# Optimization experiments

Measured on AMD Instinct MI355X. Metric: run time of the kernel, lower is better.

The kernel has to match this reference:

```python
import jax, jax.numpy as jnp
import numpy as np

N_NODES = 20000
N_EDGES = 640000
D = 64        # node / edge feature dim
H = 128       # MLP hidden dim


def setup_inputs() -> dict:
    key = jax.random.key(0)
    ks = jax.random.split(key, 12)
    inp = {
        "x": jax.random.normal(ks[0], (N_NODES, D), dtype=jnp.float32),
        "edge_index": jax.random.randint(ks[1], (2, N_EDGES), 0, N_NODES, dtype=jnp.int64),
        "edge_attr": jax.random.normal(ks[2], (N_EDGES, D), dtype=jnp.float32),
        "f": jax.random.normal(ks[3], (N_NODES, D), dtype=jnp.float32),
        # edge MLP: concat(x_src, x_dest, edge_attr) = 3D -> H -> D
        "We1": jax.random.normal(ks[4], (3 * D, H), dtype=jnp.float32) / np.sqrt(3 * D),
        "be1": jnp.zeros((H,), dtype=jnp.float32),
        "We2": jax.random.normal(ks[5], (H, D), dtype=jnp.float32) / np.sqrt(H),
        "be2": jnp.zeros((D,), dtype=jnp.float32),
        # node MLP: concat(x, agg, f) = 3D -> H -> D
        "Wn1": jax.random.normal(ks[6], (3 * D, H), dtype=jnp.float32) / np.sqrt(3 * D),
        "bn1": jnp.zeros((H,), dtype=jnp.float32),
        "Wn2": jax.random.normal(ks[7], (H, D), dtype=jnp.float32) / np.sqrt(H),
        "bn2": jnp.zeros((D,), dtype=jnp.float32),
    }
    return inp


def reference(x, edge_index, edge_attr, f, We1, be1, We2, be2, Wn1, bn1, Wn2, bn2):
    src, dest = edge_index[0], edge_index[1]
    # edge model: MLP over gathered src/dest node features + edge attrs
    e_in = jnp.concatenate([x[src], x[dest], edge_attr], axis=-1)      # [E, 3D]
    e_h = jax.nn.relu(e_in @ We1 + be1)                                 # [E, H]
    edge_out = e_h @ We2 + be2                                          # [E, D]
    # node model: scatter-add edge messages to dest, then MLP
    agg = jax.ops.segment_sum(edge_out, dest, num_segments=N_NODES)    # [N, D]
    n_in = jnp.concatenate([x, agg, f], axis=-1)                        # [N, 3D]
    n_h = jax.nn.relu(n_in @ Wn1 + bn1)                                 # [N, H]
    x_out = n_h @ Wn2 + bn2                                             # [N, D]
    return (x_out, edge_out)
```

## Files before the change

### kernel.cpp

```cpp
#include <hip/hip_runtime.h>

#define NE 640000
#define NN 20000
#define SEI 200
#define SEH 136
#define SEO 68

typedef __attribute__((ext_vector_type(8))) short s16x8;
typedef __attribute__((ext_vector_type(4))) short s16x4;
typedef __attribute__((ext_vector_type(4))) float f32x4;

typedef const __attribute__((ext_vector_type(4))) float cf32x4;

__device__ __forceinline__ short f2bf(float f) {
  unsigned int u = __float_as_uint(f);
  u += 0x7fffu + ((u >> 16) & 1u);
  return (short)(u >> 16);
}

__device__ __forceinline__ s16x8 cvt8(f32x4 a, f32x4 b) {
  s16x8 o;
  o[0]=f2bf(a[0]); o[1]=f2bf(a[1]); o[2]=f2bf(a[2]); o[3]=f2bf(a[3]);
  o[4]=f2bf(b[0]); o[5]=f2bf(b[1]); o[6]=f2bf(b[2]); o[7]=f2bf(b[3]);
  return o;
}

__device__ __forceinline__ void load_wfrags_lds(const float* W1, const float* W2,
                                                const float* b1, const float* b2,
                                                short* smem, int t,
                                                int wv, int r, int g,
                                                s16x8 w1f[2][6], s16x8 w2f[4],
                                                f32x4 b1r[2], f32x4* b2r) {
  #pragma unroll
  for (int i = 0; i < 24; ++i) {
    int idx4 = t + i * 256;
    f32x4 v = ((cf32x4*)W1)[idx4];
    s16x4 pk; pk[0]=f2bf(v[0]); pk[1]=f2bf(v[1]); pk[2]=f2bf(v[2]); pk[3]=f2bf(v[3]);
    *(s16x4*)&smem[idx4 * 4] = pk;
  }
  __syncthreads();
  #pragma unroll
  for (int nn = 0; nn < 2; ++nn) {
    const int h = (wv*2+nn)*16 + r;
    #pragma unroll
    for (int kk = 0; kk < 6; ++kk) {
      s16x8 wf;
      #pragma unroll
      for (int i = 0; i < 8; ++i) wf[i] = smem[(kk*32 + g*8 + i)*128 + h];
      w1f[nn][kk] = wf;
    }
    b1r[nn] = *(cf32x4*)(b1 + (wv*2+nn)*16 + g*4);
  }
  __syncthreads();
  #pragma unroll
  for (int i = 0; i < 8; ++i) {
    int idx4 = t + i * 256;
    f32x4 v = ((cf32x4*)W2)[idx4];
    s16x4 pk; pk[0]=f2bf(v[0]); pk[1]=f2bf(v[1]); pk[2]=f2bf(v[2]); pk[3]=f2bf(v[3]);
    *(s16x4*)&smem[idx4 * 4] = pk;
  }
  __syncthreads();
  {
    const int h2 = wv*16 + r;
    #pragma unroll
    for (int kk = 0; kk < 4; ++kk) {
      s16x8 wf;
      #pragma unroll
      for (int i = 0; i < 8; ++i) wf[i] = smem[(kk*32 + g*8 + i)*64 + h2];
      w2f[kk] = wf;
    }
    *b2r = *(cf32x4*)(b2 + wv*16 + g*4);
  }
  __syncthreads();
}


__global__ void count_kernel(const int* __restrict__ eidx, int* __restrict__ cursor,
                             float* __restrict__ agg) {
  const int4* d4 = (const int4*)(eidx + NE);
  int i = blockIdx.x * blockDim.x + threadIdx.x;
  if (i < NE / 4) {
    int4 d = d4[i];
    atomicAdd(&cursor[d.x], 1);
    atomicAdd(&cursor[d.y], 1);
    atomicAdd(&cursor[d.z], 1);
    atomicAdd(&cursor[d.w], 1);
  }
  if (i < NN * 64 / 8) {
    f32x4 z = {0.f, 0.f, 0.f, 0.f};
    ((f32x4*)agg)[i*2]   = z;
    ((f32x4*)agg)[i*2+1] = z;
  }
}

__global__ __launch_bounds__(1024)
void scan_kernel(int* __restrict__ cursor, int* __restrict__ offs) {
  __shared__ int cnt[20480];
  __shared__ int part[1024];
  const int t = threadIdx.x;
  for (int i = t; i < 20480; i += 1024)
    cnt[i] = (i < NN) ? cursor[i] : 0;
  __syncthreads();
  const int lo = t * 20;
  int s = 0;
  #pragma unroll
  for (int k = 0; k < 20; ++k) s += cnt[lo + k];
  part[t] = s;
  __syncthreads();
  for (int d = 1; d < 1024; d <<= 1) {
    int u = (t >= d) ? part[t - d] : 0;
    __syncthreads();
    part[t] += u;
    __syncthreads();
  }
  int run = part[t] - s;
  #pragma unroll
  for (int k = 0; k < 20; ++k) {
    int c = cnt[lo + k];
    cnt[lo + k] = run;
    run += c;
  }
  __syncthreads();
  for (int i = t; i < NN; i += 1024) {
    int v = cnt[i];
    offs[i] = v;
    cursor[i] = v;
  }
  if (t == 1023) offs[NN] = NE;
}

__global__ void scatter_kernel(const int* __restrict__ eidx,
                               int* __restrict__ cursor, int* __restrict__ elist) {
  const int4* d4 = (const int4*)(eidx + NE);
  int i = blockIdx.x * blockDim.x + threadIdx.x;
  if (i < NE / 4) {
    int4 d = d4[i];
    const int e = i * 4;
    elist[atomicAdd(&cursor[d.x], 1)] = e;
    elist[atomicAdd(&cursor[d.y], 1)] = e + 1;
    elist[atomicAdd(&cursor[d.z], 1)] = e + 2;
    elist[atomicAdd(&cursor[d.w], 1)] = e + 3;
  }
}

#define LOAD_ROWS(sv, dv, ee) do {                                        \
    cf32x4* ps_ = (cf32x4*)(x  + (size_t)(sv)*64 + p*16);                 \
    cf32x4* pd_ = (cf32x4*)(x  + (size_t)(dv)*64 + p*16);                 \
    cf32x4* pe_ = (cf32x4*)(ea + (size_t)(ee)*64 + p*16);                 \
    L[0]=ps_[0]; L[1]=ps_[1]; L[2]=ps_[2];  L[3]=ps_[3];                  \
    L[4]=pd_[0]; L[5]=pd_[1]; L[6]=pd_[2];  L[7]=pd_[3];                  \
    L[8]=pe_[0]; L[9]=pe_[1]; L[10]=pe_[2]; L[11]=pe_[3];                 \
  } while (0)

#define WRITE_EIN(buf) do {                                               \
    short* stg_ = (buf) + el*SEI + p*16;                                  \
    ((s16x8*)stg_)[0]       = cvt8(L[0], L[1]);                           \
    ((s16x8*)stg_)[1]       = cvt8(L[2], L[3]);                           \
    ((s16x8*)(stg_+64))[0]  = cvt8(L[4], L[5]);                           \
    ((s16x8*)(stg_+64))[1]  = cvt8(L[6], L[7]);                           \
    ((s16x8*)(stg_+128))[0] = cvt8(L[8], L[9]);                           \
    ((s16x8*)(stg_+128))[1] = cvt8(L[10], L[11]);                         \
  } while (0)

__global__ __launch_bounds__(256, 2)
void edge_kernel(const float* __restrict__ x, const int* __restrict__ eidx,
                 const float* __restrict__ ea, const int* __restrict__ elist,
                 const float* __restrict__ We1, const float* __restrict__ be1,
                 const float* __restrict__ We2, const float* __restrict__ be2,
                 float* __restrict__ edge_out, float* __restrict__ agg)
{
  __shared__ __align__(16) char smem[69632];
  short* sEin0 = (short*)smem;
  short* sEin1 = (short*)(smem + 25600);
  short* sEh   = (short*)(smem + 51200);
  int* sDest0  = (int*)(smem + 68608);
  int* sDest1  = (int*)(smem + 68864);
  int* sEid0   = (int*)(smem + 69120);
  int* sEid1   = (int*)(smem + 69376);

  const int t = threadIdx.x;
  const int wv = t >> 6, lane = t & 63;
  const int r = lane & 15, g = lane >> 4;

  s16x8 w1f[2][6], w2f[4];
  f32x4 b1r[2], b2r;
  load_wfrags_lds(We1, We2, be1, be2, (short*)smem, t, wv, r, g,
                  w1f, w2f, b1r, &b2r);

  const int el = t >> 2, p = t & 3;
  const int nT = NE / 64;
  const int S = (int)gridDim.x;
  const f32x4 zero = {0.f, 0.f, 0.f, 0.f};

  f32x4 L[12];
  int eW = 0, dW = 0;
  int eI = 0, sI = 0, dI = 0;
  int tile = blockIdx.x;

  if (tile < nT) {
    int e0 = elist[(tile << 6) + el];
    int s0 = eidx[e0], d0 = eidx[NE + e0];
    LOAD_ROWS(s0, d0, e0);
    WRITE_EIN(sEin0);
    if (p == 0) { sDest0[el] = d0; sEid0[el] = e0; }
    const int t1 = tile + S;
    if (t1 < nT) {
      eW = elist[(t1 << 6) + el];
      int sv = eidx[eW]; dW = eidx[NE + eW];
      LOAD_ROWS(sv, dW, eW);
    }
    const int t2 = tile + 2 * S;
    if (t2 < nT) {
      eI = elist[(t2 << 6) + el];
      sI = eidx[eI]; dI = eidx[NE + eI];
    }
  }
  __syncthreads();

  int cur = 0;
  while (tile < nT) {
    const short* Ecur = cur ? sEin1 : sEin0;
    short* Enxt = cur ? sEin0 : sEin1;
    float* EoutC = (float*)(cur ? (smem + 25600) : smem);
    const int* sDestC = cur ? sDest1 : sDest0;
    const int* sEidC  = cur ? sEid1  : sEid0;
    int* sDestN = cur ? sDest0 : sDest1;
    int* sEidN  = cur ? sEid0  : sEid1;

    const int tW = tile + S, tI = tile + 2 * S, tX = tile + 3 * S;
    if (tW < nT) {
      WRITE_EIN(Enxt);
      if (p == 0) { sDestN[el] = dW; sEidN[el] = eW; }
    }
    if (tI < nT) { LOAD_ROWS(sI, dI, eI); eW = eI; dW = dI; }
    if (tX < nT) {
      eI = elist[(tX << 6) + el];
      sI = eidx[eI]; dI = eidx[NE + eI];
    }

    f32x4 acc1[2][4];
    #pragma unroll
    for (int nn = 0; nn < 2; ++nn)
      #pragma unroll
      for (int j = 0; j < 4; ++j) acc1[nn][j] = zero;
    #pragma unroll
    for (int kk = 0; kk < 6; ++kk) {
      #pragma unroll
      for (int j = 0; j < 4; ++j) {
        s16x8 ef = *(const s16x8*)&Ecur[(j*16 + r)*SEI + kk*32 + g*8];
        acc1[0][j] = __builtin_amdgcn_mfma_f32_16x16x32_bf16(w1f[0][kk], ef, acc1[0][j], 0, 0, 0);
        acc1[1][j] = __builtin_amdgcn_mfma_f32_16x16x32_bf16(w1f[1][kk], ef, acc1[1][j], 0, 0, 0);
      }
    }
    #pragma unroll
    for (int nn = 0; nn < 2; ++nn)
      #pragma unroll
      for (int j = 0; j < 4; ++j) {
        s16x4 pk;
        #pragma unroll
        for (int q = 0; q < 4; ++q) {
          float v = acc1[nn][j][q] + b1r[nn][q];
          pk[q] = f2bf(v > 0.f ? v : 0.f);
        }
        *(s16x4*)&sEh[(j*16 + r)*SEH + (wv*2+nn)*16 + g*4] = pk;
      }
    __syncthreads();

    #pragma unroll
    for (int j = 0; j < 4; ++j) {
      f32x4 a2 = zero;
      #pragma unroll
      for (int kk = 0; kk < 4; ++kk) {
        s16x8 hf = *(const s16x8*)&sEh[(j*16 + r)*SEH + kk*32 + g*8];
        a2 = __builtin_amdgcn_mfma_f32_16x16x32_bf16(w2f[kk], hf, a2, 0, 0, 0);
      }
      a2 += b2r;
      const int eg = sEidC[j*16 + r];
      *(f32x4*)&edge_out[(size_t)eg*64 + wv*16 + g*4] = a2;
      *(f32x4*)&EoutC[(j*16 + r)*SEO + wv*16 + g*4] = a2;
    }
    __syncthreads();

    {
      const int row0 = wv * 16;
      float acc = EoutC[row0*SEO + lane];
      int dcur = sDestC[row0];
      #pragma unroll
      for (int k = 1; k < 16; ++k) {
        const int dn = sDestC[row0 + k];
        const float v = EoutC[(row0 + k)*SEO + lane];
        if (dn != dcur) {
          unsafeAtomicAdd(&agg[(size_t)dcur*64 + lane], acc);
          acc = v; dcur = dn;
        } else {
          acc += v;
        }
      }
      unsafeAtomicAdd(&agg[(size_t)dcur*64 + lane], acc);
    }
    __syncthreads();
    cur ^= 1;
    tile = tW;
  }
}

__global__ __launch_bounds__(256, 2)
void node_kernel(const float* __restrict__ x, const float* agg,
                 const float* __restrict__ f,
                 const float* __restrict__ Wn1, const float* __restrict__ bn1,
                 const float* __restrict__ Wn2, const float* __restrict__ bn2,
                 float* x_out)
{
  __shared__ __align__(16) char smem[49152];
  short* sEin = (short*)smem;
  short* sEh  = (short*)(smem + 25600);

  const int t = threadIdx.x;
  const int wv = t >> 6, lane = t & 63;
  const int r = lane & 15, g = lane >> 4;

  s16x8 w1f[2][6], w2f[4];
  f32x4 b1r[2], b2r;
  load_wfrags_lds(Wn1, Wn2, bn1, bn2, (short*)smem, t, wv, r, g,
                  w1f, w2f, b1r, &b2r);

  const int el = t >> 2, p = t & 3;
  const f32x4 zero = {0.f, 0.f, 0.f, 0.f};
  const int nT = (NN + 63) / 64;

  for (int tile = blockIdx.x; tile < nT; tile += (int)gridDim.x) {
    const int base = tile << 6;
    const int i = base + el;

    f32x4 L[12];
    if (i < NN) {
      cf32x4* ps_ = (cf32x4*)(x   + (size_t)i*64 + p*16);
      cf32x4* pa_ = (cf32x4*)(agg + (size_t)i*64 + p*16);
      cf32x4* pf_ = (cf32x4*)(f   + (size_t)i*64 + p*16);
      L[0]=ps_[0]; L[1]=ps_[1]; L[2]=ps_[2];  L[3]=ps_[3];
      L[4]=pa_[0]; L[5]=pa_[1]; L[6]=pa_[2];  L[7]=pa_[3];
      L[8]=pf_[0]; L[9]=pf_[1]; L[10]=pf_[2]; L[11]=pf_[3];
    } else {
      #pragma unroll
      for (int q = 0; q < 12; ++q) L[q] = zero;
    }
    WRITE_EIN(sEin);
    __syncthreads();

    f32x4 acc1[2][4];
    #pragma unroll
    for (int nn = 0; nn < 2; ++nn)
      #pragma unroll
      for (int j = 0; j < 4; ++j) acc1[nn][j] = zero;
    #pragma unroll
    for (int kk = 0; kk < 6; ++kk) {
      #pragma unroll
      for (int j = 0; j < 4; ++j) {
        s16x8 ef = *(const s16x8*)&sEin[(j*16 + r)*SEI + kk*32 + g*8];
        acc1[0][j] = __builtin_amdgcn_mfma_f32_16x16x32_bf16(w1f[0][kk], ef, acc1[0][j], 0, 0, 0);
        acc1[1][j] = __builtin_amdgcn_mfma_f32_16x16x32_bf16(w1f[1][kk], ef, acc1[1][j], 0, 0, 0);
      }
    }
    #pragma unroll
    for (int nn = 0; nn < 2; ++nn)
      #pragma unroll
      for (int j = 0; j < 4; ++j) {
        s16x4 pk;
        #pragma unroll
        for (int q = 0; q < 4; ++q) {
          float v = acc1[nn][j][q] + b1r[nn][q];
          pk[q] = f2bf(v > 0.f ? v : 0.f);
        }
        *(s16x4*)&sEh[(j*16 + r)*SEH + (wv*2+nn)*16 + g*4] = pk;
      }
    __syncthreads();

    #pragma unroll
    for (int j = 0; j < 4; ++j) {
      f32x4 a2 = zero;
      #pragma unroll
      for (int kk = 0; kk < 4; ++kk) {
        s16x8 hf = *(const s16x8*)&sEh[(j*16 + r)*SEH + kk*32 + g*8];
        a2 = __builtin_amdgcn_mfma_f32_16x16x32_bf16(w2f[kk], hf, a2, 0, 0, 0);
      }
      const int row = base + j*16 + r;
      if (row < NN) {
        f32x4 v = a2 + b2r;
        *(f32x4*)&x_out[(size_t)row*64 + wv*16 + g*4] = v;
      }
    }
    __syncthreads();
  }
}

extern "C" void kernel_launch(void* const* d_in, const int* in_sizes, int n_in,
                              void* d_out, int out_size, void* d_ws, size_t ws_size,
                              hipStream_t stream) {
  const float* x   = (const float*)d_in[0];
  const int*   ei  = (const int*)d_in[1];
  const float* ea  = (const float*)d_in[2];
  const float* f   = (const float*)d_in[3];
  const float* We1 = (const float*)d_in[4];
  const float* be1 = (const float*)d_in[5];
  const float* We2 = (const float*)d_in[6];
  const float* be2 = (const float*)d_in[7];
  const float* Wn1 = (const float*)d_in[8];
  const float* bn1 = (const float*)d_in[9];
  const float* Wn2 = (const float*)d_in[10];
  const float* bn2 = (const float*)d_in[11];

  float* x_out    = (float*)d_out;
  float* edge_out = x_out + (size_t)NN * 64;

  int* cursor = (int*)d_ws;
  int* offs   = cursor + NN;
  int* elist  = offs + NN + 8;

  hipMemsetAsync(cursor, 0, NN * sizeof(int), stream);
  count_kernel<<<625, 256, 0, stream>>>(ei, cursor, x_out);
  scan_kernel<<<1, 1024, 0, stream>>>(cursor, offs);
  scatter_kernel<<<625, 256, 0, stream>>>(ei, cursor, elist);
  edge_kernel<<<512, 256, 0, stream>>>(x, ei, ea, elist, We1, be1, We2, be2,
                                       edge_out, x_out);
  node_kernel<<<105, 256, 0, stream>>>(x, x_out, f, Wn1, bn1, Wn2, bn2, x_out);
}
```

Baseline: 223.8 us.

## Fuse whole pipeline into one cooperative persistent kernel with grid syncs

```diff
diff --git a/kernel.cpp b/kernel.cpp
--- a/kernel.cpp
+++ b/kernel.cpp
@@ -1,4 +1,7 @@
 #include <hip/hip_runtime.h>
+#include <hip/hip_cooperative_groups.h>
+
+namespace cg = cooperative_groups;
 
 #define NE 640000
 #define NN 20000
@@ -72,6 +75,332 @@
     *b2r = *(cf32x4*)(b2 + wv*16 + g*4);
   }
   __syncthreads();
+}
+
+#define LOAD_ROWS(sv, dv, ee) do {                                        \
+    cf32x4* ps_ = (cf32x4*)(x  + (size_t)(sv)*64 + p*16);                 \
+    cf32x4* pd_ = (cf32x4*)(x  + (size_t)(dv)*64 + p*16);                 \
+    cf32x4* pe_ = (cf32x4*)(ea + (size_t)(ee)*64 + p*16);                 \
+    L[0]=ps_[0]; L[1]=ps_[1]; L[2]=ps_[2];  L[3]=ps_[3];                  \
+    L[4]=pd_[0]; L[5]=pd_[1]; L[6]=pd_[2];  L[7]=pd_[3];                  \
+    L[8]=pe_[0]; L[9]=pe_[1]; L[10]=pe_[2]; L[11]=pe_[3];                 \
+  } while (0)
+
+#define WRITE_EIN(buf) do {                                               \
+    short* stg_ = (buf) + el*SEI + p*16;                                  \
+    ((s16x8*)stg_)[0]       = cvt8(L[0], L[1]);                           \
+    ((s16x8*)stg_)[1]       = cvt8(L[2], L[3]);                           \
+    ((s16x8*)(stg_+64))[0]  = cvt8(L[4], L[5]);                           \
+    ((s16x8*)(stg_+64))[1]  = cvt8(L[6], L[7]);                           \
+    ((s16x8*)(stg_+128))[0] = cvt8(L[8], L[9]);                           \
+    ((s16x8*)(stg_+128))[1] = cvt8(L[10], L[11]);                         \
+  } while (0)
+
+__global__ __launch_bounds__(256, 2)
+void fused_kernel(const float* __restrict__ x, const int* __restrict__ eidx,
+                  const float* __restrict__ ea, const float* __restrict__ f,
+                  const float* __restrict__ We1, const float* __restrict__ be1,
+                  const float* __restrict__ We2, const float* __restrict__ be2,
+                  const float* __restrict__ Wn1, const float* __restrict__ bn1,
+                  const float* __restrict__ Wn2, const float* __restrict__ bn2,
+                  float* __restrict__ edge_out, float* agg,
+                  int* cursor, int* offs, int* elist, int* bsum)
+{
+  cg::grid_group grid = cg::this_grid();
+  __shared__ __align__(16) char smem[69632];
+
+  const int t = threadIdx.x;
+  const int bid = (int)blockIdx.x;
+  const int nB = (int)gridDim.x;
+  const int gtid = bid * 256 + t;
+  const int gsz = nB * 256;
+
+  for (int i = gtid; i < NN; i += gsz) cursor[i] = 0;
+  {
+    f32x4 z = {0.f, 0.f, 0.f, 0.f};
+    for (int i = gtid; i < NN * 16; i += gsz) ((f32x4*)agg)[i] = z;
+  }
+  grid.sync();
+
+  {
+    const int4* d4 = (const int4*)(eidx + NE);
+    for (int i = gtid; i < NE / 4; i += gsz) {
+      int4 d = d4[i];
+      atomicAdd(&cursor[d.x], 1);
+      atomicAdd(&cursor[d.y], 1);
+      atomicAdd(&cursor[d.z], 1);
+      atomicAdd(&cursor[d.w], 1);
+    }
+  }
+  grid.sync();
+
+  const int CH = (NN + nB - 1) / nB;
+  const int lo = bid * CH;
+  {
+    int* red  = (int*)smem;
+    int* cbuf = red + 256;
+    int myc = 0;
+    if (t < CH && lo + t < NN) myc = cursor[lo + t];
+    red[t] = myc;
+    __syncthreads();
+    #pragma unroll
+    for (int d = 128; d > 0; d >>= 1) {
+      if (t < d) red[t] += red[t + d];
+      __syncthreads();
+    }
+    if (t == 0) bsum[bid] = red[0];
+    grid.sync();
+    int pb = 0;
+    for (int i = t; i < bid; i += 256) pb += bsum[i];
+    red[t] = pb;
+    __syncthreads();
+    #pragma unroll
+    for (int d = 128; d > 0; d >>= 1) {
+      if (t < d) red[t] += red[t + d];
+      __syncthreads();
+    }
+    const int base = red[0];
+    __syncthreads();
+    cbuf[t] = myc;
+    __syncthreads();
+    for (int dd = 1; dd < 256; dd <<= 1) {
+      int u = (t >= dd) ? cbuf[t - dd] : 0;
+      __syncthreads();
+      cbuf[t] += u;
+      __syncthreads();
+    }
+    if (t < CH && lo + t < NN) {
+      int run = base + cbuf[t] - myc;
+      offs[lo + t] = run;
+      cursor[lo + t] = run;
+    }
+    if (bid == 0 && t == 0) offs[NN] = NE;
+  }
+  grid.sync();
+
+  {
+    const int4* d4 = (const int4*)(eidx + NE);
+    for (int i = gtid; i < NE / 4; i += gsz) {
+      int4 d = d4[i];
+      const int e = i * 4;
+      elist[atomicAdd(&cursor[d.x], 1)] = e;
+      elist[atomicAdd(&cursor[d.y], 1)] = e + 1;
+      elist[atomicAdd(&cursor[d.z], 1)] = e + 2;
+      elist[atomicAdd(&cursor[d.w], 1)] = e + 3;
+    }
+  }
+  grid.sync();
+
+  const int wv = t >> 6, lane = t & 63;
+  const int r = lane & 15, g = lane >> 4;
+  const int el = t >> 2, p = t & 3;
+
+  {
+    short* sEin0 = (short*)smem;
+    short* sEin1 = (short*)(smem + 25600);
+    short* sEh   = (short*)(smem + 51200);
+    int* sDest0  = (int*)(smem + 68608);
+    int* sDest1  = (int*)(smem + 68864);
+    int* sEid0   = (int*)(smem + 69120);
+    int* sEid1   = (int*)(smem + 69376);
+
+    s16x8 w1f[2][6], w2f[4];
+    f32x4 b1r[2], b2r;
+    load_wfrags_lds(We1, We2, be1, be2, (short*)smem, t, wv, r, g,
+                    w1f, w2f, b1r, &b2r);
+
+    const int nT = NE / 64;
+    const int S = nB;
+    const f32x4 zero = {0.f, 0.f, 0.f, 0.f};
+
+    f32x4 L[12];
+    int eW = 0, dW = 0, eI = 0, sI = 0, dI = 0;
+    int tile = bid;
+
+    if (tile < nT) {
+      int e0 = elist[(tile << 6) + el];
+      int s0 = eidx[e0], d0 = eidx[NE + e0];
+      LOAD_ROWS(s0, d0, e0);
+      WRITE_EIN(sEin0);
+      if (p == 0) { sDest0[el] = d0; sEid0[el] = e0; }
+      const int t1 = tile + S;
+      if (t1 < nT) {
+        eW = elist[(t1 << 6) + el];
+        int sv = eidx[eW]; dW = eidx[NE + eW];
+        LOAD_ROWS(sv, dW, eW);
+      }
+      const int t2 = tile + 2 * S;
+      if (t2 < nT) {
+        eI = elist[(t2 << 6) + el];
+        sI = eidx[eI]; dI = eidx[NE + eI];
+      }
+    }
+    __syncthreads();
+
+    int cur = 0;
+    while (tile < nT) {
+      const short* Ecur = cur ? sEin1 : sEin0;
+      short* Enxt = cur ? sEin0 : sEin1;
+      float* EoutC = (float*)(cur ? (smem + 25600) : smem);
+      const int* sDestC = cur ? sDest1 : sDest0;
+      const int* sEidC  = cur ? sEid1  : sEid0;
+      int* sDestN = cur ? sDest0 : sDest1;
+      int* sEidN  = cur ? sEid0  : sEid1;
+
+      const int tW = tile + S, tI = tile + 2 * S, tX = tile + 3 * S;
+      if (tW < nT) {
+        WRITE_EIN(Enxt);
+        if (p == 0) { sDestN[el] = dW; sEidN[el] = eW; }
+      }
+      if (tI < nT) { LOAD_ROWS(sI, dI, eI); eW = eI; dW = dI; }
+      if (tX < nT) {
+        eI = elist[(tX << 6) + el];
+        sI = eidx[eI]; dI = eidx[NE + eI];
+      }
+
+      f32x4 acc1[2][4];
+      #pragma unroll
+      for (int nn = 0; nn < 2; ++nn)
+        #pragma unroll
+        for (int j = 0; j < 4; ++j) acc1[nn][j] = zero;
+      #pragma unroll
+      for (int kk = 0; kk < 6; ++kk) {
+        #pragma unroll
+        for (int j = 0; j < 4; ++j) {
+          s16x8 ef = *(const s16x8*)&Ecur[(j*16 + r)*SEI + kk*32 + g*8];
+          acc1[0][j] = __builtin_amdgcn_mfma_f32_16x16x32_bf16(w1f[0][kk], ef, acc1[0][j], 0, 0, 0);
+          acc1[1][j] = __builtin_amdgcn_mfma_f32_16x16x32_bf16(w1f[1][kk], ef, acc1[1][j], 0, 0, 0);
+        }
+      }
+      #pragma unroll
+      for (int nn = 0; nn < 2; ++nn)
+        #pragma unroll
+        for (int j = 0; j < 4; ++j) {
+          s16x4 pk;
+          #pragma unroll
+          for (int q = 0; q < 4; ++q) {
+            float v = acc1[nn][j][q] + b1r[nn][q];
+            pk[q] = f2bf(v > 0.f ? v : 0.f);
+          }
+          *(s16x4*)&sEh[(j*16 + r)*SEH + (wv*2+nn)*16 + g*4] = pk;
+        }
+      __syncthreads();
+
+      #pragma unroll
+      for (int j = 0; j < 4; ++j) {
+        f32x4 a2 = zero;
+        #pragma unroll
+        for (int kk = 0; kk < 4; ++kk) {
+          s16x8 hf = *(const s16x8*)&sEh[(j*16 + r)*SEH + kk*32 + g*8];
+          a2 = __builtin_amdgcn_mfma_f32_16x16x32_bf16(w2f[kk], hf, a2, 0, 0, 0);
+        }
+        a2 += b2r;
+        const int eg = sEidC[j*16 + r];
+        *(f32x4*)&edge_out[(size_t)eg*64 + wv*16 + g*4] = a2;
+        *(f32x4*)&EoutC[(j*16 + r)*SEO + wv*16 + g*4] = a2;
+      }
+      __syncthreads();
+
+      {
+        const int row0 = wv * 16;
+        float acc = EoutC[row0*SEO + lane];
+        int dcur = sDestC[row0];
+        #pragma unroll
+        for (int k = 1; k < 16; ++k) {
+          const int dn = sDestC[row0 + k];
+          const float v = EoutC[(row0 + k)*SEO + lane];
+          if (dn != dcur) {
+            unsafeAtomicAdd(&agg[(size_t)dcur*64 + lane], acc);
+            acc = v; dcur = dn;
+          } else {
+            acc += v;
+          }
+        }
+        unsafeAtomicAdd(&agg[(size_t)dcur*64 + lane], acc);
+      }
+      __syncthreads();
+      cur ^= 1;
+      tile = tW;
+    }
+  }
+  grid.sync();
+
+  {
+    short* sEin = (short*)smem;
+    short* sEh  = (short*)(smem + 25600);
+
+    s16x8 w1f[2][6], w2f[4];
+    f32x4 b1r[2], b2r;
+    load_wfrags_lds(Wn1, Wn2, bn1, bn2, (short*)smem, t, wv, r, g,
+                    w1f, w2f, b1r, &b2r);
+
+    const f32x4 zero = {0.f, 0.f, 0.f, 0.f};
+    const int nTn = (NN + 63) / 64;
+
+    for (int tile = bid; tile < nTn; tile += nB) {
+      const int base = tile << 6;
+      const int i = base + el;
+
+      f32x4 L[12];
+      if (i < NN) {
+        cf32x4* ps_ = (cf32x4*)(x   + (size_t)i*64 + p*16);
+        cf32x4* pa_ = (cf32x4*)(agg + (size_t)i*64 + p*16);
+        cf32x4* pf_ = (cf32x4*)(f   + (size_t)i*64 + p*16);
+        L[0]=ps_[0]; L[1]=ps_[1]; L[2]=ps_[2];  L[3]=ps_[3];
+        L[4]=pa_[0]; L[5]=pa_[1]; L[6]=pa_[2];  L[7]=pa_[3];
+        L[8]=pf_[0]; L[9]=pf_[1]; L[10]=pf_[2]; L[11]=pf_[3];
+      } else {
+        #pragma unroll
+        for (int q = 0; q < 12; ++q) L[q] = zero;
+      }
+      WRITE_EIN(sEin);
+      __syncthreads();
+
+      f32x4 acc1[2][4];
+      #pragma unroll
+      for (int nn = 0; nn < 2; ++nn)
+        #pragma unroll
+        for (int j = 0; j < 4; ++j) acc1[nn][j] = zero;
+      #pragma unroll
+      for (int kk = 0; kk < 6; ++kk) {
+        #pragma unroll
+        for (int j = 0; j < 4; ++j) {
+          s16x8 ef = *(const s16x8*)&sEin[(j*16 + r)*SEI + kk*32 + g*8];
+          acc1[0][j] = __builtin_amdgcn_mfma_f32_16x16x32_bf16(w1f[0][kk], ef, acc1[0][j], 0, 0, 0);
+          acc1[1][j] = __builtin_amdgcn_mfma_f32_16x16x32_bf16(w1f[1][kk], ef, acc1[1][j], 0, 0, 0);
+        }
+      }
+      #pragma unroll
+      for (int nn = 0; nn < 2; ++nn)
+        #pragma unroll
+        for (int j = 0; j < 4; ++j) {
+          s16x4 pk;
+          #pragma unroll
+          for (int q = 0; q < 4; ++q) {
+            float v = acc1[nn][j][q] + b1r[nn][q];
+            pk[q] = f2bf(v > 0.f ? v : 0.f);
+          }
+          *(s16x4*)&sEh[(j*16 + r)*SEH + (wv*2+nn)*16 + g*4] = pk;
+        }
+      __syncthreads();
+
+      #pragma unroll
+      for (int j = 0; j < 4; ++j) {
+        f32x4 a2 = zero;
+        #pragma unroll
+        for (int kk = 0; kk < 4; ++kk) {
+          s16x8 hf = *(const s16x8*)&sEh[(j*16 + r)*SEH + kk*32 + g*8];
+          a2 = __builtin_amdgcn_mfma_f32_16x16x32_bf16(w2f[kk], hf, a2, 0, 0, 0);
+        }
+        const int row = base + j*16 + r;
+        if (row < NN) {
+          f32x4 v = a2 + b2r;
+          *(f32x4*)&agg[(size_t)row*64 + wv*16 + g*4] = v;
+        }
+      }
+      __syncthreads();
+    }
+  }
 }
 
 
@@ -143,25 +472,6 @@
   }
 }
 
-#define LOAD_ROWS(sv, dv, ee) do {                                        \
-    cf32x4* ps_ = (cf32x4*)(x  + (size_t)(sv)*64 + p*16);                 \
-    cf32x4* pd_ = (cf32x4*)(x  + (size_t)(dv)*64 + p*16);                 \
-    cf32x4* pe_ = (cf32x4*)(ea + (size_t)(ee)*64 + p*16);                 \
-    L[0]=ps_[0]; L[1]=ps_[1]; L[2]=ps_[2];  L[3]=ps_[3];                  \
-    L[4]=pd_[0]; L[5]=pd_[1]; L[6]=pd_[2];  L[7]=pd_[3];                  \
-    L[8]=pe_[0]; L[9]=pe_[1]; L[10]=pe_[2]; L[11]=pe_[3];                 \
-  } while (0)
-
-#define WRITE_EIN(buf) do {                                               \
-    short* stg_ = (buf) + el*SEI + p*16;                                  \
-    ((s16x8*)stg_)[0]       = cvt8(L[0], L[1]);                           \
-    ((s16x8*)stg_)[1]       = cvt8(L[2], L[3]);                           \
-    ((s16x8*)(stg_+64))[0]  = cvt8(L[4], L[5]);                           \
-    ((s16x8*)(stg_+64))[1]  = cvt8(L[6], L[7]);                           \
-    ((s16x8*)(stg_+128))[0] = cvt8(L[8], L[9]);                           \
-    ((s16x8*)(stg_+128))[1] = cvt8(L[10], L[11]);                         \
-  } while (0)
-
 __global__ __launch_bounds__(256, 2)
 void edge_kernel(const float* __restrict__ x, const int* __restrict__ eidx,
                  const float* __restrict__ ea, const int* __restrict__ elist,
@@ -415,6 +725,19 @@
   int* cursor = (int*)d_ws;
   int* offs   = cursor + NN;
   int* elist  = offs + NN + 8;
+  int* bsum   = elist + NE + 8;
+
+  void* args[] = {
+    (void*)&x, (void*)&ei, (void*)&ea, (void*)&f,
+    (void*)&We1, (void*)&be1, (void*)&We2, (void*)&be2,
+    (void*)&Wn1, (void*)&bn1, (void*)&Wn2, (void*)&bn2,
+    (void*)&edge_out, (void*)&x_out,
+    (void*)&cursor, (void*)&offs, (void*)&elist, (void*)&bsum
+  };
+  hipError_t err = hipLaunchCooperativeKernel((void*)fused_kernel,
+                                              dim3(512), dim3(256),
+                                              args, 0, stream);
+  if (err == hipSuccess) return;
 
   hipMemsetAsync(cursor, 0, NN * sizeof(int), stream);
   count_kernel<<<625, 256, 0, stream>>>(ei, cursor, x_out);
```

Result: slower. 564.1 us (+152.0%).
